# Kernel optimization log

Measured on AMD Instinct MI355X. Metric: run time of the kernel, lower is better.

Reference implementation:

```python
import jax, jax.numpy as jnp
import numpy as np

D_MODEL = 1024
D_INNER = 2 * D_MODEL          # expand=2
D_STATE = 16
D_CONV = 4
DT_RANK = D_MODEL // 16        # ceil(1024/16)
BATCH, SEQ = 4, 1024
LN_EPS = 1e-5
LRELU_SLOPE = 0.01


def setup_inputs() -> dict:
    key = jax.random.key(0)
    ks = jax.random.split(key, 12)
    s = 0.02
    return {
        "x": jax.random.normal(ks[0], (BATCH, SEQ, D_MODEL), jnp.float32),
        "W_in": jax.random.normal(ks[1], (D_MODEL, 2 * D_INNER), jnp.float32) * s,
        "conv_w": jax.random.normal(ks[2], (D_INNER, D_CONV), jnp.float32) * s,
        "conv_b": jnp.zeros((D_INNER,), jnp.float32),
        "W_x": jax.random.normal(ks[3], (D_INNER, DT_RANK + 2 * D_STATE), jnp.float32) * s,
        "W_dt": jax.random.normal(ks[4], (DT_RANK, D_INNER), jnp.float32) * s,
        "b_dt": jax.random.normal(ks[5], (D_INNER,), jnp.float32) * 0.1 - 4.0,
        "A_log": jnp.log(jnp.broadcast_to(jnp.arange(1, D_STATE + 1, dtype=jnp.float32), (D_INNER, D_STATE))),
        "D": jnp.ones((D_INNER,), jnp.float32),
        "W_out": jax.random.normal(ks[6], (D_INNER, D_MODEL), jnp.float32) * s,
        "gamma": jnp.ones((D_MODEL,), jnp.float32),
        "beta": jnp.zeros((D_MODEL,), jnp.float32),
    }


def _selective_scan(u, dt, A, B, C, Dp):
    # u, dt: (b, l, d); A: (d, n); B, C: (b, l, n); Dp: (d,)
    dA = jnp.exp(dt[..., None] * A)                       # (b, l, d, n)
    dBu = dt[..., None] * B[:, :, None, :] * u[..., None]  # (b, l, d, n)

    def step(h, inp):
        dA_t, dBu_t, C_t = inp                            # (b,d,n),(b,d,n),(b,n)
        h = dA_t * h + dBu_t
        y = jnp.einsum("bdn,bn->bd", h, C_t)
        return h, y

    h0 = jnp.zeros((u.shape[0], u.shape[2], A.shape[1]), u.dtype)
    xs = (dA.transpose(1, 0, 2, 3), dBu.transpose(1, 0, 2, 3), C.transpose(1, 0, 2))
    _, ys = jax.lax.scan(step, h0, xs)                    # ys: (l, b, d)
    return ys.transpose(1, 0, 2) + u * Dp                 # (b, l, d)


def _mamba(x, W_in, conv_w, conv_b, W_x, W_dt, b_dt, A_log, Dp, W_out):
    xz = x @ W_in                                          # (b, l, 2*di)
    xc, z = jnp.split(xz, 2, axis=-1)
    # causal depthwise conv over time
    xc_t = xc.transpose(0, 2, 1)                           # (b, di, l)
    kern = conv_w[:, None, :]                              # (di, 1, k)
    conv = jax.lax.conv_general_dilated(
        xc_t, kern, window_strides=(1,), padding=[(D_CONV - 1, 0)],
        dimension_numbers=("NCH", "OIH", "NCH"), feature_group_count=D_INNER)
    xc = jax.nn.silu(conv + conv_b[None, :, None]).transpose(0, 2, 1)  # (b, l, di)

    x_dbl = xc @ W_x                                       # (b, l, dt_rank + 2n)
    dt, Bm, Cm = jnp.split(x_dbl, [DT_RANK, DT_RANK + D_STATE], axis=-1)
    dt = jax.nn.softplus(dt @ W_dt + b_dt)                 # (b, l, di)
    A = -jnp.exp(A_log)                                    # (di, n)

    y = _selective_scan(xc, dt, A, Bm, Cm, Dp)             # (b, l, di)
    y = y * jax.nn.silu(z)
    return y @ W_out                                       # (b, l, d_model)


def reference(x, W_in, conv_w, conv_b, W_x, W_dt, b_dt, A_log, D, W_out, gamma, beta):
    h = x + _mamba(x, W_in, conv_w, conv_b, W_x, W_dt, b_dt, A_log, D, W_out)
    mu = jnp.mean(h, axis=-1, keepdims=True)
    var = jnp.mean(jnp.square(h - mu), axis=-1, keepdims=True)
    h = (h - mu) * jax.lax.rsqrt(var + LN_EPS) * gamma + beta
    return jnp.where(h >= 0, h, LRELU_SLOPE * h)
```

## Files before the change

kernel.cpp:

```cpp
#include <hip/hip_runtime.h>
#include <hip/hip_fp16.h>
#include <cstdint>
#include <cstddef>

typedef _Float16 f16x8 __attribute__((ext_vector_type(8)));
typedef _Float16 f16x4 __attribute__((ext_vector_type(4)));
typedef float    f32x4 __attribute__((ext_vector_type(4)));

#define TC  64
#define NCH 16

__device__ __forceinline__ float sigmoidf_(float x) { return 1.f / (1.f + __expf(-x)); }

__device__ __forceinline__ void gload_lds16(const _Float16* g, _Float16* l) {
  __builtin_amdgcn_global_load_lds(
      (const __attribute__((address_space(1))) void*)g,
      (__attribute__((address_space(3))) void*)l, 16, 0, 0);
}

__device__ __forceinline__ void t16_body(const float* __restrict__ src,
    _Float16* __restrict__ dst, int R, int C, int Cpad, int bx, int by,
    int tid, float tile[32][33]) {
  int c0 = bx * 32, r0 = by * 32, tx = tid & 31, ty = tid >> 5;
  #pragma unroll
  for (int i = 0; i < 4; ++i) {
    int r = r0 + ty + i * 8, c = c0 + tx;
    tile[ty + i * 8][tx] = (r < R && c < C) ? src[(size_t)r * C + c] : 0.f;
  }
  __syncthreads();
  #pragma unroll
  for (int i = 0; i < 4; ++i) {
    int cc = c0 + ty + i * 8, rr = r0 + tx;
    if (cc < Cpad && rr < R) dst[(size_t)cc * R + rr] = (_Float16)tile[tx][ty + i * 8];
  }
}

__global__ __launch_bounds__(256) void k_prep(
    const float* __restrict__ x, _Float16* __restrict__ x16,
    const float* __restrict__ W_in, _Float16* __restrict__ WinT,
    const float* __restrict__ W_x, _Float16* __restrict__ WxT,
    const float* __restrict__ W_dt, _Float16* __restrict__ WdtT,
    const float* __restrict__ W_out, _Float16* __restrict__ WoutT,
    const float* __restrict__ convw, _Float16* __restrict__ cwT)
{
  __shared__ float tile[32][33];
  const int blk = blockIdx.x, tid = threadIdx.x;
  if (blk < 4096) {
    int i = blk * 256 + tid;
    float4 v = ((const float4*)x)[i];
    f16x4 o = {(_Float16)v.x, (_Float16)v.y, (_Float16)v.z, (_Float16)v.w};
    ((f16x4*)x16)[i] = o;
  } else if (blk < 8192) {
    int b = blk - 4096;
    t16_body(W_in, WinT, 1024, 4096, 4096, b & 127, b >> 7, tid, tile);
  } else if (blk < 8448) {
    int b = blk - 8192;
    t16_body(W_x, WxT, 2048, 96, 128, b & 3, b >> 2, tid, tile);
  } else if (blk < 8576) {
    int b = blk - 8448;
    t16_body(W_dt, WdtT, 64, 2048, 2048, b & 63, b >> 6, tid, tile);
  } else if (blk < 10624) {
    int b = blk - 8576;
    t16_body(W_out, WoutT, 2048, 1024, 1024, b & 31, b >> 5, tid, tile);
  } else {
    #pragma unroll
    for (int j = 0; j < 32; ++j) {
      int idx = j * 256 + tid;
      int tap = idx >> 11, d = idx & 2047;
      cwT[idx] = (_Float16)convw[d * 4 + tap];
    }
  }
}

template <int EPI>
__global__ __launch_bounds__(256) void k_gemm_bt(
    const _Float16* __restrict__ A,
    const _Float16* __restrict__ BT,
    float* __restrict__ C,
    _Float16* __restrict__ C16,
    _Float16* __restrict__ AUX,
    const float* __restrict__ bias,
    int M, int N, int K)
{
  __shared__ __align__(16) _Float16 As[128 * 64];
  __shared__ __align__(16) _Float16 Bs[128 * 64];
  const int tid  = threadIdx.x;
  const int lane = tid & 63;
  const int wave = tid >> 6;
  const int wm = (wave >> 1) * 64;
  const int wn = (wave & 1) * 64;
  const int l15 = lane & 15;
  const int q   = lane >> 4;
  const int m0 = blockIdx.y * 128;
  const int n0 = blockIdx.x * 128;

  const int kpb = K / gridDim.z;
  const int k0  = blockIdx.z * kpb;

  const int rch = lane >> 3;
  const int g   = (lane & 7) ^ (rch & 7);
  const _Float16* gA = A  + (size_t)(m0 + wave * 32 + rch) * K + k0 + g * 8;
  const _Float16* gB = BT + (size_t)(n0 + wave * 32 + rch) * K + k0 + g * 8;
  _Float16* lA = As + wave * 32 * 64 + lane * 8;
  _Float16* lB = Bs + wave * 32 * 64 + lane * 8;

  const int sx = l15 & 7;

  f32x4 acc[4][4] = {};

  for (int k = 0; k < kpb; k += 64) {
    #pragma unroll
    for (int c = 0; c < 4; ++c) {
      gload_lds16(gA + (size_t)(c * 8) * K + k, lA + c * 512);
      gload_lds16(gB + (size_t)(c * 8) * K + k, lB + c * 512);
    }
    __syncthreads();
    #pragma unroll
    for (int k32 = 0; k32 < 2; ++k32) {
      f16x8 af[4], bf[4];
      #pragma unroll
      for (int i = 0; i < 4; ++i) {
        af[i] = *(const f16x8*)&As[(wm + i * 16 + l15) * 64 + ((k32 * 4 + q) ^ sx) * 8];
        bf[i] = *(const f16x8*)&Bs[(wn + i * 16 + l15) * 64 + ((k32 * 4 + q) ^ sx) * 8];
      }
      #pragma unroll
      for (int mi = 0; mi < 4; ++mi)
        #pragma unroll
        for (int ni = 0; ni < 4; ++ni)
          acc[mi][ni] = __builtin_amdgcn_mfma_f32_16x16x32_f16(af[mi], bf[ni], acc[mi][ni], 0, 0, 0);
    }
    __syncthreads();
  }

  #pragma unroll
  for (int mi = 0; mi < 4; ++mi) {
    #pragma unroll
    for (int ni = 0; ni < 4; ++ni) {
      int col = n0 + wn + ni * 16 + l15;
      #pragma unroll
      for (int r = 0; r < 4; ++r) {
        int row = m0 + wm + mi * 16 + q * 4 + r;
        float v = acc[mi][ni][r];
        if constexpr (EPI == 2) {
          float t = v + bias[col];
          float sp = (t > 20.f) ? t : log1pf(__expf(t));
          AUX[(size_t)row * N + col] = (_Float16)sp;
        } else if constexpr (EPI == 3) {
          if (col < 2048) {
            C16[(size_t)row * 2048 + col] = (_Float16)v;
          } else {
            AUX[(size_t)row * 2048 + (col - 2048)] = (_Float16)(v * sigmoidf_(v));
          }
        } else {
          C[(size_t)blockIdx.z * M * N + (size_t)row * N + col] = v;
        }
      }
    }
  }
}

__global__ __launch_bounds__(256) void k_red(const float* __restrict__ Cp,
                                             _Float16* __restrict__ dtin,
                                             float* __restrict__ xbc) {
  int i = blockIdx.x * 256 + threadIdx.x;
  const int PL = 4096 * 128;
  float s = Cp[i] + Cp[i + PL] + Cp[i + 2 * PL] + Cp[i + 3 * PL];
  int col = i & 127, row = i >> 7;
  if (col < 64) dtin[(size_t)row * 64 + col] = (_Float16)s;
  else if (col < 96) xbc[(size_t)row * 32 + (col - 64)] = s;
}

__global__ __launch_bounds__(256) void k_conv_silu(
    const _Float16* __restrict__ xc, const _Float16* __restrict__ cwT,
    const float* __restrict__ cb, _Float16* __restrict__ out)
{
  const int row = blockIdx.x;
  const int t = row & 1023;
  const int d8 = threadIdx.x;
  const size_t base = (size_t)row * 2048 + d8 * 8;
  f16x8 p0 = *(const f16x8*)&xc[base];
  f16x8 w3 = *(const f16x8*)&cwT[3 * 2048 + d8 * 8];
  float4 cb0 = ((const float4*)cb)[d8 * 2];
  float4 cb1 = ((const float4*)cb)[d8 * 2 + 1];
  float accv[8] = {cb0.x, cb0.y, cb0.z, cb0.w, cb1.x, cb1.y, cb1.z, cb1.w};
  #pragma unroll
  for (int j = 0; j < 8; ++j) accv[j] += (float)w3[j] * (float)p0[j];
  if (t >= 1) {
    f16x8 p = *(const f16x8*)&xc[base - 2048];
    f16x8 w = *(const f16x8*)&cwT[2 * 2048 + d8 * 8];
    #pragma unroll
    for (int j = 0; j < 8; ++j) accv[j] += (float)w[j] * (float)p[j];
  }
  if (t >= 2) {
    f16x8 p = *(const f16x8*)&xc[base - 4096];
    f16x8 w = *(const f16x8*)&cwT[1 * 2048 + d8 * 8];
    #pragma unroll
    for (int j = 0; j < 8; ++j) accv[j] += (float)w[j] * (float)p[j];
  }
  if (t >= 3) {
    f16x8 p = *(const f16x8*)&xc[base - 6144];
    f16x8 w = *(const f16x8*)&cwT[0 * 2048 + d8 * 8];
    #pragma unroll
    for (int j = 0; j < 8; ++j) accv[j] += (float)w[j] * (float)p[j];
  }
  f16x8 o;
  #pragma unroll
  for (int j = 0; j < 8; ++j) o[j] = (_Float16)(accv[j] * sigmoidf_(accv[j]));
  *(f16x8*)&out[base] = o;
}

__global__ __launch_bounds__(256) void k_scan_part(
    const _Float16* __restrict__ dt, const _Float16* __restrict__ u,
    const float* __restrict__ xbc, const float* __restrict__ A_log,
    float* __restrict__ P, float* __restrict__ S)
{
  const int tid = threadIdx.x;
  const int d = blockIdx.x * 256 + tid;
  const int c = blockIdx.y;
  const int b = blockIdx.z;
  const int row0 = b * 1024 + c * TC;
  __shared__ float Bs[TC * 16];
  for (int i = tid; i < TC * 16; i += 256) {
    int t = i >> 4, n = i & 15;
    Bs[i] = xbc[(size_t)(row0 + t) * 32 + n];
  }
  float a[16];
  #pragma unroll
  for (int n = 0; n < 16; ++n) a[n] = -__expf(A_log[d * 16 + n]);
  float h[16] = {};
  float sumdt = 0.f;
  __syncthreads();
  for (int t = 0; t < TC; ++t) {
    const int row = row0 + t;
    float dtv = (float)dt[(size_t)row * 2048 + d];
    float uv  = (float)u[(size_t)row * 2048 + d];
    float dtu = dtv * uv;
    sumdt += dtv;
    #pragma unroll
    for (int n = 0; n < 16; ++n)
      h[n] = h[n] * __expf(dtv * a[n]) + dtu * Bs[t * 16 + n];
  }
  const size_t base = (size_t)(b * NCH + c) * 16 * 2048 + d;
  #pragma unroll
  for (int n = 0; n < 16; ++n) {
    P[base + n * 2048] = __expf(sumdt * a[n]);
    S[base + n * 2048] = h[n];
  }
}

__global__ __launch_bounds__(256) void k_scan_comb(
    float* __restrict__ P, const float* __restrict__ S)
{
  int idx = blockIdx.x * 256 + threadIdx.x;
  int d = idx & 2047;
  int n = (idx >> 11) & 15;
  int b = idx >> 15;
  float H = 0.f;
  for (int c = 0; c < NCH - 1; ++c) {
    size_t off = ((size_t)(b * NCH + c) * 16 + n) * 2048 + d;
    H = P[off] * H + S[off];
    P[off] = H;
  }
}

__global__ __launch_bounds__(256) void k_scan_y(
    const _Float16* dt, const _Float16* __restrict__ u,
    const _Float16* __restrict__ zs, const float* __restrict__ xbc,
    const float* __restrict__ A_log, const float* __restrict__ Hbuf,
    const float* __restrict__ Dv, _Float16* ys)
{
  const int tid = threadIdx.x;
  const int d = blockIdx.x * 256 + tid;
  const int c = blockIdx.y;
  const int b = blockIdx.z;
  const int row0 = b * 1024 + c * TC;
  __shared__ float Bs[TC * 16], Cs[TC * 16];
  for (int i = tid; i < TC * 16; i += 256) {
    int t = i >> 4, n = i & 15;
    Bs[i] = xbc[(size_t)(row0 + t) * 32 + n];
    Cs[i] = xbc[(size_t)(row0 + t) * 32 + 16 + n];
  }
  float a[16];
  #pragma unroll
  for (int n = 0; n < 16; ++n) a[n] = -__expf(A_log[d * 16 + n]);
  float h[16];
  if (c == 0) {
    #pragma unroll
    for (int n = 0; n < 16; ++n) h[n] = 0.f;
  } else {
    const size_t hb = (size_t)(b * NCH + (c - 1)) * 16 * 2048 + d;
    #pragma unroll
    for (int n = 0; n < 16; ++n) h[n] = Hbuf[hb + n * 2048];
  }
  const float Dd = Dv[d];
  __syncthreads();
  for (int t = 0; t < TC; ++t) {
    const int row = row0 + t;
    float dtv = (float)dt[(size_t)row * 2048 + d];
    float uv  = (float)u[(size_t)row * 2048 + d];
    float zv  = (float)zs[(size_t)row * 2048 + d];
    float dtu = dtv * uv;
    float y = uv * Dd;
    #pragma unroll
    for (int n = 0; n < 16; ++n) {
      h[n] = h[n] * __expf(dtv * a[n]) + dtu * Bs[t * 16 + n];
      y = fmaf(h[n], Cs[t * 16 + n], y);
    }
    ys[(size_t)row * 2048 + d] = (_Float16)(y * zv);
  }
}

__global__ __launch_bounds__(256) void k_resid_ln(
    const float* __restrict__ x, const float* __restrict__ yp,
    const float* __restrict__ gamma, const float* __restrict__ beta,
    float* __restrict__ out)
{
  int row = blockIdx.x;
  int tid = threadIdx.x;
  const int PL4 = 4096 * 256;
  const int o4 = row * 256 + tid;
  float4 xv = ((const float4*)x)[o4];
  float4 p0 = ((const float4*)yp)[o4];
  float4 p1 = ((const float4*)yp)[o4 + PL4];
  float4 p2 = ((const float4*)yp)[o4 + 2 * PL4];
  float4 p3 = ((const float4*)yp)[o4 + 3 * PL4];
  float v[4] = {xv.x + p0.x + p1.x + p2.x + p3.x,
                xv.y + p0.y + p1.y + p2.y + p3.y,
                xv.z + p0.z + p1.z + p2.z + p3.z,
                xv.w + p0.w + p1.w + p2.w + p3.w};
  float s = v[0] + v[1] + v[2] + v[3];
  float s2 = v[0]*v[0] + v[1]*v[1] + v[2]*v[2] + v[3]*v[3];
  #pragma unroll
  for (int off = 32; off > 0; off >>= 1) {
    s  += __shfl_down(s, off, 64);
    s2 += __shfl_down(s2, off, 64);
  }
  __shared__ float rs[4], rs2[4];
  int wv = tid >> 6, ln = tid & 63;
  if (ln == 0) { rs[wv] = s; rs2[wv] = s2; }
  __syncthreads();
  if (tid == 0) {
    float a = 0.f, b2 = 0.f;
    #pragma unroll
    for (int i = 0; i < 4; ++i) { a += rs[i]; b2 += rs2[i]; }
    rs[0] = a; rs2[0] = b2;
  }
  __syncthreads();
  float mu  = rs[0] * (1.f / 1024.f);
  float var = rs2[0] * (1.f / 1024.f) - mu * mu;
  float inv = rsqrtf(var + 1e-5f);
  float4 gv = ((const float4*)gamma)[tid];
  float4 bv = ((const float4*)beta)[tid];
  float gg[4] = {gv.x, gv.y, gv.z, gv.w};
  float bb[4] = {bv.x, bv.y, bv.z, bv.w};
  float4 ov;
  float* op = (float*)&ov;
  #pragma unroll
  for (int i = 0; i < 4; ++i) {
    float hn = (v[i] - mu) * inv * gg[i] + bb[i];
    op[i] = hn >= 0.f ? hn : 0.01f * hn;
  }
  ((float4*)out)[o4] = ov;
}

extern "C" void kernel_launch(void* const* d_in, const int* in_sizes, int n_in,
                              void* d_out, int out_size, void* d_ws, size_t ws_size,
                              hipStream_t stream)
{
  const float* x     = (const float*)d_in[0];
  const float* W_in  = (const float*)d_in[1];
  const float* convw = (const float*)d_in[2];
  const float* convb = (const float*)d_in[3];
  const float* W_x   = (const float*)d_in[4];
  const float* W_dt  = (const float*)d_in[5];
  const float* b_dt  = (const float*)d_in[6];
  const float* A_log = (const float*)d_in[7];
  const float* Dv    = (const float*)d_in[8];
  const float* W_out = (const float*)d_in[9];
  const float* gamma = (const float*)d_in[10];
  const float* beta  = (const float*)d_in[11];
  float* out = (float*)d_out;

  char* ws = (char*)d_ws;
  const size_t MB = 1ull << 20;
  _Float16* x16   = (_Float16*)(ws + 0 * MB);
  _Float16* WinT  = (_Float16*)(ws + 8 * MB);
  _Float16* xc16  = (_Float16*)(ws + 16 * MB);
  _Float16* zsil  = (_Float16*)(ws + 32 * MB);
  _Float16* xcs   = (_Float16*)(ws + 48 * MB);
  _Float16* dtb   = (_Float16*)(ws + 64 * MB);
  _Float16* WxT   = (_Float16*)(ws + 80 * MB);
  _Float16* WdtT  = (_Float16*)(ws + 80 * MB + 512 * 1024);
  _Float16* WoutT = (_Float16*)(ws + 81 * MB);
  float*    Cpart = (float*)   (ws + 85 * MB);
  float*    xbc   = (float*)   (ws + 93 * MB);
  _Float16* dtin  = (_Float16*)(ws + 93 * MB + 512 * 1024);
  _Float16* cwT   = (_Float16*)(ws + 94 * MB);
  float*    Pb    = (float*)   (ws + 0 * MB);
  float*    Sb    = (float*)   (ws + 8 * MB);
  _Float16* ysb   = dtb;
  float*    yp    = (float*)   (ws + 0 * MB);

  k_prep<<<10625, 256, 0, stream>>>(x, x16, W_in, WinT, W_x, WxT, W_dt, WdtT,
                                    W_out, WoutT, convw, cwT);
  k_gemm_bt<3><<<dim3(32, 32), 256, 0, stream>>>(x16, WinT, nullptr, xc16, zsil, nullptr, 4096, 4096, 1024);
  k_conv_silu<<<4096, 256, 0, stream>>>(xc16, cwT, convb, xcs);
  k_gemm_bt<4><<<dim3(1, 32, 4), 256, 0, stream>>>(xcs, WxT, Cpart, nullptr, nullptr, nullptr, 4096, 128, 2048);
  k_red<<<4096 * 128 / 256, 256, 0, stream>>>(Cpart, dtin, xbc);
  k_gemm_bt<2><<<dim3(16, 32), 256, 0, stream>>>(dtin, WdtT, nullptr, nullptr, dtb, b_dt, 4096, 2048, 64);
  k_scan_part<<<dim3(8, NCH, 4), 256, 0, stream>>>(dtb, xcs, xbc, A_log, Pb, Sb);
  k_scan_comb<<<4 * 16 * 2048 / 256, 256, 0, stream>>>(Pb, Sb);
  k_scan_y<<<dim3(8, NCH, 4), 256, 0, stream>>>(dtb, xcs, zsil, xbc, A_log, Pb, Dv, ysb);
  k_gemm_bt<4><<<dim3(8, 32, 4), 256, 0, stream>>>(ysb, WoutT, yp, nullptr, nullptr, nullptr, 4096, 1024, 2048);
  k_resid_ln<<<4096, 256, 0, stream>>>(x, yp, gamma, beta, out);
}
```

Baseline: 372.5 us.

## Stage GEMM epilogues through LDS for vectorized fp16 stores; halve out-proj split-K

The fp16-output GEMM epilogues (softplus dt, in-proj split with SiLU) now write each wave's 16x64 tile to LDS and store it to global memory as 16-byte vectors instead of scattered 2-byte stores. The output projection drops from 4-way to 2-way split-K and writes fp16 partials through a new epilogue variant. The residual LayerNorm kernel reads two fp16 partials instead of four fp32 ones. This cuts store transactions and partial-buffer traffic, at the cost of fewer blocks in the out-proj GEMM, extra barriers in the epilogue, and fp16 rounding of the partial sums.

Result: faster. 364.7 us (-2.1%).

```diff
diff --git a/kernel.cpp b/kernel.cpp
--- a/kernel.cpp
+++ b/kernel.cpp
@@ -132,29 +132,68 @@
     __syncthreads();
   }
 
-  #pragma unroll
-  for (int mi = 0; mi < 4; ++mi) {
-    #pragma unroll
-    for (int ni = 0; ni < 4; ++ni) {
-      int col = n0 + wn + ni * 16 + l15;
+  if constexpr (EPI == 4) {
+    #pragma unroll
+    for (int mi = 0; mi < 4; ++mi) {
       #pragma unroll
-      for (int r = 0; r < 4; ++r) {
-        int row = m0 + wm + mi * 16 + q * 4 + r;
-        float v = acc[mi][ni][r];
-        if constexpr (EPI == 2) {
-          float t = v + bias[col];
-          float sp = (t > 20.f) ? t : log1pf(__expf(t));
-          AUX[(size_t)row * N + col] = (_Float16)sp;
-        } else if constexpr (EPI == 3) {
-          if (col < 2048) {
-            C16[(size_t)row * 2048 + col] = (_Float16)v;
-          } else {
-            AUX[(size_t)row * 2048 + (col - 2048)] = (_Float16)(v * sigmoidf_(v));
-          }
-        } else {
-          C[(size_t)blockIdx.z * M * N + (size_t)row * N + col] = v;
+      for (int ni = 0; ni < 4; ++ni) {
+        int col = n0 + wn + ni * 16 + l15;
+        #pragma unroll
+        for (int r = 0; r < 4; ++r) {
+          int row = m0 + wm + mi * 16 + q * 4 + r;
+          C[(size_t)blockIdx.z * M * N + (size_t)row * N + col] = acc[mi][ni][r];
         }
       }
+    }
+  } else {
+    _Float16* Ep = As + wave * 1280;
+    const int rr = lane >> 2, cb = lane & 3;
+    #pragma unroll
+    for (int mi = 0; mi < 4; ++mi) {
+      #pragma unroll
+      for (int ni = 0; ni < 4; ++ni) {
+        int col = n0 + wn + ni * 16 + l15;
+        #pragma unroll
+        for (int r = 0; r < 4; ++r) {
+          float v = acc[mi][ni][r];
+          _Float16 hv;
+          if constexpr (EPI == 2) {
+            float t = v + bias[col];
+            float sp = (t > 20.f) ? t : log1pf(__expf(t));
+            hv = (_Float16)sp;
+          } else if constexpr (EPI == 3) {
+            hv = (n0 >= 2048) ? (_Float16)(v * sigmoidf_(v)) : (_Float16)v;
+          } else {
+            hv = (_Float16)v;
+          }
+          Ep[(q * 4 + r) * 72 + ni * 16 + l15] = hv;
+        }
+      }
+      __syncthreads();
+      f16x8 o0 = *(const f16x8*)&Ep[rr * 72 + cb * 16];
+      f16x8 o1 = *(const f16x8*)&Ep[rr * 72 + cb * 16 + 8];
+      int row = m0 + wm + mi * 16 + rr;
+      int colb = wn + cb * 16;
+      if constexpr (EPI == 2) {
+        _Float16* dst = AUX + (size_t)row * N + n0 + colb;
+        *(f16x8*)dst = o0;
+        *(f16x8*)(dst + 8) = o1;
+      } else if constexpr (EPI == 3) {
+        if (n0 < 2048) {
+          _Float16* dst = C16 + (size_t)row * 2048 + n0 + colb;
+          *(f16x8*)dst = o0;
+          *(f16x8*)(dst + 8) = o1;
+        } else {
+          _Float16* dst = AUX + (size_t)row * 2048 + (n0 - 2048) + colb;
+          *(f16x8*)dst = o0;
+          *(f16x8*)(dst + 8) = o1;
+        }
+      } else {
+        _Float16* dst = C16 + (size_t)blockIdx.z * M * N + (size_t)row * N + n0 + colb;
+        *(f16x8*)dst = o0;
+        *(f16x8*)(dst + 8) = o1;
+      }
+      __syncthreads();
     }
   }
 }
@@ -311,23 +350,21 @@
 }
 
 __global__ __launch_bounds__(256) void k_resid_ln(
-    const float* __restrict__ x, const float* __restrict__ yp,
+    const float* __restrict__ x, const _Float16* __restrict__ yp,
     const float* __restrict__ gamma, const float* __restrict__ beta,
     float* __restrict__ out)
 {
   int row = blockIdx.x;
   int tid = threadIdx.x;
-  const int PL4 = 4096 * 256;
+  const int PLH = 4096 * 1024;
   const int o4 = row * 256 + tid;
   float4 xv = ((const float4*)x)[o4];
-  float4 p0 = ((const float4*)yp)[o4];
-  float4 p1 = ((const float4*)yp)[o4 + PL4];
-  float4 p2 = ((const float4*)yp)[o4 + 2 * PL4];
-  float4 p3 = ((const float4*)yp)[o4 + 3 * PL4];
-  float v[4] = {xv.x + p0.x + p1.x + p2.x + p3.x,
-                xv.y + p0.y + p1.y + p2.y + p3.y,
-                xv.z + p0.z + p1.z + p2.z + p3.z,
-                xv.w + p0.w + p1.w + p2.w + p3.w};
+  f16x4 a0 = ((const f16x4*)yp)[o4];
+  f16x4 a1 = ((const f16x4*)(yp + PLH))[o4];
+  float v[4] = {xv.x + (float)a0[0] + (float)a1[0],
+                xv.y + (float)a0[1] + (float)a1[1],
+                xv.z + (float)a0[2] + (float)a1[2],
+                xv.w + (float)a0[3] + (float)a1[3]};
   float s = v[0] + v[1] + v[2] + v[3];
   float s2 = v[0]*v[0] + v[1]*v[1] + v[2]*v[2] + v[3]*v[3];
   #pragma unroll
@@ -399,7 +436,7 @@
   float*    Pb    = (float*)   (ws + 0 * MB);
   float*    Sb    = (float*)   (ws + 8 * MB);
   _Float16* ysb   = dtb;
-  float*    yp    = (float*)   (ws + 0 * MB);
+  _Float16* ypH   = (_Float16*)(ws + 0 * MB);
 
   k_prep<<<10625, 256, 0, stream>>>(x, x16, W_in, WinT, W_x, WxT, W_dt, WdtT,
                                     W_out, WoutT, convw, cwT);
@@ -411,6 +448,6 @@
   k_scan_part<<<dim3(8, NCH, 4), 256, 0, stream>>>(dtb, xcs, xbc, A_log, Pb, Sb);
   k_scan_comb<<<4 * 16 * 2048 / 256, 256, 0, stream>>>(Pb, Sb);
   k_scan_y<<<dim3(8, NCH, 4), 256, 0, stream>>>(dtb, xcs, zsil, xbc, A_log, Pb, Dv, ysb);
-  k_gemm_bt<4><<<dim3(8, 32, 4), 256, 0, stream>>>(ysb, WoutT, yp, nullptr, nullptr, nullptr, 4096, 1024, 2048);
-  k_resid_ln<<<4096, 256, 0, stream>>>(x, yp, gamma, beta, out);
-}
+  k_gemm_bt<5><<<dim3(8, 32, 2), 256, 0, stream>>>(ysb, WoutT, nullptr, ypH, nullptr, nullptr, 4096, 1024, 2048);
+  k_resid_ln<<<4096, 256, 0, stream>>>(x, ypH, gamma, beta, out);
+}
```
